# Kernel tuning notes

Hardware: AMD Instinct MI355X
Metric: run time of the kernel (lower is better)

## Reference

```python
import jax, jax.numpy as jnp
import numpy as np

N_NODES = 100000
N_EDGES = 1600000
N_FEAT = 128
HIDDEN = 64
N_CLASSES = 16


def setup_inputs() -> dict:
    key = jax.random.key(0)
    ks = jax.random.split(key, 8)
    x = jax.random.normal(ks[0], (N_NODES, N_FEAT), dtype=jnp.float32)
    edge_index = jax.random.randint(ks[1], (2, N_EDGES), 0, N_NODES, dtype=jnp.int64)
    def glorot(k, shape):
        lim = float(np.sqrt(6.0 / (shape[0] + shape[1])))
        return jax.random.uniform(k, shape, jnp.float32, -lim, lim)
    return {
        "x": x,
        "edge_index": edge_index,
        "W0": glorot(ks[2], (N_FEAT, HIDDEN)), "b0": jnp.zeros((HIDDEN,), jnp.float32),
        "W1": glorot(ks[3], (HIDDEN, HIDDEN)), "b1": jnp.zeros((HIDDEN,), jnp.float32),
        "W2": glorot(ks[4], (HIDDEN, 2)),      "b2": jnp.zeros((2,), jnp.float32),
        "Wc": glorot(ks[5], (2, N_CLASSES)),   "bc": jnp.zeros((N_CLASSES,), jnp.float32),
    }


def _gcn_conv(x, W, b, src, dst, norm, n_nodes):
    # GCNConv: D^{-1/2} (A + I) D^{-1/2} X W + b, edges already include self-loops
    h = x @ W                                  # transform first (small dim)
    msg = h[src] * norm[:, None]               # gather + per-edge scale
    agg = jax.ops.segment_sum(msg, dst, num_segments=n_nodes)  # scatter-add
    return agg + b


def reference(x, edge_index, W0, b0, W1, b1, W2, b2, Wc, bc):
    n = x.shape[0]
    loops = jnp.arange(n, dtype=edge_index.dtype)
    src = jnp.concatenate([edge_index[0], loops])
    dst = jnp.concatenate([edge_index[1], loops])
    # degree on destination (col), including self-loops
    deg = jax.ops.segment_sum(jnp.ones_like(dst, dtype=x.dtype), dst, num_segments=n)
    dis = jnp.where(deg > 0, jax.lax.rsqrt(deg), 0.0)
    norm = dis[src] * dis[dst]

    h = _gcn_conv(x, W0, b0, src, dst, norm, n)              # layer 0, no activation
    h = jnp.tanh(_gcn_conv(h, W1, b1, src, dst, norm, n))    # layer 1
    h = jnp.tanh(_gcn_conv(h, W2, b2, src, dst, norm, n))    # layer 2 -> [N, 2]
    embeddings = h
    out = embeddings @ Wc + bc                               # [N, num_classes]
    return (out, embeddings)
```

## Files before the change

kernel.cpp:

```cpp
#include <hip/hip_runtime.h>


#define NF 128
#define NH 64
#define NPB 256
#define MAXNB 512
#define CAP 6144
#define A1G 1024

typedef _Float16 half8 __attribute__((ext_vector_type(8)));
typedef float f32x4 __attribute__((ext_vector_type(4)));

__global__ void k_init0(const int* __restrict__ ei, int* __restrict__ fmt,
                        int* __restrict__ ccnt, int nb16) {
    int i = blockIdx.x * 256 + threadIdx.x;
    if (i < nb16) ccnt[i] = 0;
    if (i == 0) {
        int f = 1;
        #pragma unroll
        for (int k = 1; k < 32; k += 2) if (ei[k] != 0) f = 0;
        *fmt = f;
    }
}

__global__ void __launch_bounds__(256) k_coarse(
        const int* __restrict__ ei, const int* __restrict__ fmt,
        int* __restrict__ ccnt, int* __restrict__ blockbase, int E, int NB) {
    __shared__ int h[MAXNB];
    int sh = *fmt;
    for (int i = threadIdx.x; i < NB; i += 256) h[i] = 0;
    __syncthreads();
    for (long long e = (long long)blockIdx.x * 256 + threadIdx.x; e < E;
         e += (long long)A1G * 256) {
        int d = ei[(long long)(E + e) << sh];
        atomicAdd(&h[d >> 8], 1);
    }
    __syncthreads();
    for (int b = threadIdx.x; b < NB; b += 256) {
        int c = h[b];
        int base = (c > 0) ? atomicAdd(&ccnt[b * 16], c) : 0;
        blockbase[(long long)blockIdx.x * NB + b] = base;
    }
}

__global__ void __launch_bounds__(512) k_cscan(
        const int* __restrict__ ccnt, int* __restrict__ cstart, int NB) {
    __shared__ int s[512];
    int t = threadIdx.x;
    int c = (t < NB) ? ccnt[t * 16] : 0;
    s[t] = c;
    __syncthreads();
    for (int off = 1; off < 512; off <<= 1) {
        int v = s[t];
        int u = (t >= off) ? s[t - off] : 0;
        __syncthreads();
        s[t] = v + u;
        __syncthreads();
    }
    if (t < NB) cstart[t] = s[t] - c;
}

__global__ void __launch_bounds__(256) k_cscatter(
        const int* __restrict__ ei, const int* __restrict__ fmt,
        const int* __restrict__ cstart, const int* __restrict__ blockbase,
        int* __restrict__ pairs, int E, int NB) {
    __shared__ int h[MAXNB];
    __shared__ int bb[MAXNB];
    int sh = *fmt;
    for (int i = threadIdx.x; i < NB; i += 256) {
        h[i] = 0;
        bb[i] = cstart[i] + blockbase[(long long)blockIdx.x * NB + i];
    }
    __syncthreads();
    for (long long e = (long long)blockIdx.x * 256 + threadIdx.x; e < E;
         e += (long long)A1G * 256) {
        int s = ei[(long long)e << sh];
        int d = ei[(long long)(E + e) << sh];
        int b = d >> 8;
        int r = atomicAdd(&h[b], 1);
        pairs[bb[b] + r] = s | ((d & 255) << 17);
    }
}

__global__ void __launch_bounds__(256) k_bucket(
        const int* __restrict__ pairs, const int* __restrict__ ccnt,
        const int* __restrict__ cstart, int* __restrict__ esrc,
        int* __restrict__ cnt, int* __restrict__ start, float* __restrict__ dis,
        int N) {
    __shared__ int words[CAP];
    __shared__ unsigned char rk[CAP];
    __shared__ int h[NPB];
    __shared__ int hs[NPB];
    int b = blockIdx.x;
    int cs = cstart[b];
    int ec = ccnt[b * 16];
    if (ec > CAP) ec = CAP;
    int t = threadIdx.x;
    for (int i = t; i < ec; i += 256) words[i] = pairs[cs + i];
    h[t] = 0;
    __syncthreads();
    for (int i = t; i < ec; i += 256) {
        int ld = words[i] >> 17;
        rk[i] = (unsigned char)atomicAdd(&h[ld], 1);
    }
    __syncthreads();
    int c = h[t];
    hs[t] = c;
    __syncthreads();
    for (int off = 1; off < 256; off <<= 1) {
        int v = hs[t];
        int u = (t >= off) ? hs[t - off] : 0;
        __syncthreads();
        hs[t] = v + u;
        __syncthreads();
    }
    int node = b * NPB + t;
    if (node < N) {
        cnt[node] = c;
        start[node] = cs + hs[t] - c;
        dis[node] = rsqrtf(1.0f + (float)c);
    }
    for (int i = t; i < ec; i += 256) {
        int w = words[i];
        int ld = w >> 17;
        esrc[cs + (hs[ld] - h[ld]) + rk[i]] = w & 0x1FFFF;
    }
}

__global__ void k_wprep(const float* __restrict__ W, short* __restrict__ wf) {
    int b = blockIdx.x;
    int kc = b >> 2, ct = b & 3;
    int t = threadIdx.x;
    int lane = t & 63;
    int j0 = (t >> 6) * 2;
    #pragma unroll
    for (int jj = 0; jj < 2; ++jj) {
        int j = j0 + jj;
        int k = kc * 32 + (lane >> 4) * 8 + j;
        int col = ct * 16 + (lane & 15);
        float w = W[k * NH + col];
        _Float16 h = (_Float16)w;
        _Float16 l = (_Float16)(w - (float)h);
        int idx = (b * 64 + lane) * 8 + j;
        wf[idx] = *(short*)&h;
        wf[idx + 8192] = *(short*)&l;
    }
}

#define KPX 68
__global__ void __launch_bounds__(256) k_gemmM(
        const float* __restrict__ X, const short* __restrict__ wfrag,
        const float* __restrict__ dis, short* __restrict__ T16,
        float* __restrict__ rs, int n) {
    __shared__ __align__(16) short Wf[16384];
    __shared__ __align__(16) float xs[64 * KPX];
    int tid = threadIdx.x;
    {
        const int4* src = (const int4*)wfrag;
        int4* dst = (int4*)Wf;
        #pragma unroll
        for (int u = 0; u < 8; ++u) dst[tid + u * 256] = src[tid + u * 256];
    }
    long long rowbase = (long long)blockIdx.x * 64;
    int lane = tid & 63;
    int wid = tid >> 6;
    f32x4 acc0 = {0,0,0,0}, acc1 = {0,0,0,0}, acc2 = {0,0,0,0}, acc3 = {0,0,0,0};
    #pragma unroll
    for (int ph = 0; ph < 2; ++ph) {
        __syncthreads();
        const float* Xp = X + rowbase * NF + ph * 64;
        #pragma unroll
        for (int u = 0; u < 4; ++u) {
            int i = tid + u * 256;
            int r = i >> 4, kk = (i & 15) << 2;
            float4 v = (rowbase + r < n)
                           ? *(const float4*)(Xp + r * NF + kk)
                           : make_float4(0.f, 0.f, 0.f, 0.f);
            *(float4*)&xs[r * KPX + kk] = v;
        }
        __syncthreads();
        #pragma unroll
        for (int kcl = 0; kcl < 2; ++kcl) {
            const float* xp =
                &xs[(wid * 16 + (lane & 15)) * KPX + kcl * 32 + (lane >> 4) * 8];
            float4 xa = *(const float4*)xp;
            float4 xb = *(const float4*)(xp + 4);
            float xv[8] = {xa.x, xa.y, xa.z, xa.w, xb.x, xb.y, xb.z, xb.w};
            half8 ah, al;
            #pragma unroll
            for (int e = 0; e < 8; ++e) {
                _Float16 h = (_Float16)xv[e];
                ah[e] = h;
                al[e] = (_Float16)(xv[e] - (float)h);
            }
            int kc = ph * 2 + kcl;
            {
                const half8 bh = *(const half8*)&Wf[((kc * 4 + 0) * 64 + lane) * 8];
                const half8 bl = *(const half8*)&Wf[((kc * 4 + 0) * 64 + lane) * 8 + 8192];
                acc0 = __builtin_amdgcn_mfma_f32_16x16x32_f16(ah, bh, acc0, 0, 0, 0);
                acc0 = __builtin_amdgcn_mfma_f32_16x16x32_f16(ah, bl, acc0, 0, 0, 0);
                acc0 = __builtin_amdgcn_mfma_f32_16x16x32_f16(al, bh, acc0, 0, 0, 0);
            }
            {
                const half8 bh = *(const half8*)&Wf[((kc * 4 + 1) * 64 + lane) * 8];
                const half8 bl = *(const half8*)&Wf[((kc * 4 + 1) * 64 + lane) * 8 + 8192];
                acc1 = __builtin_amdgcn_mfma_f32_16x16x32_f16(ah, bh, acc1, 0, 0, 0);
                acc1 = __builtin_amdgcn_mfma_f32_16x16x32_f16(ah, bl, acc1, 0, 0, 0);
                acc1 = __builtin_amdgcn_mfma_f32_16x16x32_f16(al, bh, acc1, 0, 0, 0);
            }
            {
                const half8 bh = *(const half8*)&Wf[((kc * 4 + 2) * 64 + lane) * 8];
                const half8 bl = *(const half8*)&Wf[((kc * 4 + 2) * 64 + lane) * 8 + 8192];
                acc2 = __builtin_amdgcn_mfma_f32_16x16x32_f16(ah, bh, acc2, 0, 0, 0);
                acc2 = __builtin_amdgcn_mfma_f32_16x16x32_f16(ah, bl, acc2, 0, 0, 0);
                acc2 = __builtin_amdgcn_mfma_f32_16x16x32_f16(al, bh, acc2, 0, 0, 0);
            }
            {
                const half8 bh = *(const half8*)&Wf[((kc * 4 + 3) * 64 + lane) * 8];
                const half8 bl = *(const half8*)&Wf[((kc * 4 + 3) * 64 + lane) * 8 + 8192];
                acc3 = __builtin_amdgcn_mfma_f32_16x16x32_f16(ah, bh, acc3, 0, 0, 0);
                acc3 = __builtin_amdgcn_mfma_f32_16x16x32_f16(ah, bl, acc3, 0, 0, 0);
                acc3 = __builtin_amdgcn_mfma_f32_16x16x32_f16(al, bh, acc3, 0, 0, 0);
            }
        }
    }
    int rb = (int)rowbase + wid * 16 + (lane >> 4) * 4;
    float dr0 = (rb + 0 < n) ? dis[rb + 0] : 0.0f;
    float dr1 = (rb + 1 < n) ? dis[rb + 1] : 0.0f;
    float dr2 = (rb + 2 < n) ? dis[rb + 2] : 0.0f;
    float dr3 = (rb + 3 < n) ? dis[rb + 3] : 0.0f;
    float drs[4] = {dr0, dr1, dr2, dr3};
    const float ks = 1.0f / 32767.0f;
    int cb = lane & 15;
    #pragma unroll
    for (int r = 0; r < 4; ++r) {
        float v0 = acc0[r] * drs[r];
        float v1 = acc1[r] * drs[r];
        float v2 = acc2[r] * drs[r];
        float v3 = acc3[r] * drs[r];
        float m = fmaxf(fmaxf(fabsf(v0), fabsf(v1)), fmaxf(fabsf(v2), fabsf(v3)));
        m = fmaxf(m, __shfl_xor(m, 1, 64));
        m = fmaxf(m, __shfl_xor(m, 2, 64));
        m = fmaxf(m, __shfl_xor(m, 4, 64));
        m = fmaxf(m, __shfl_xor(m, 8, 64));
        float ir = 32767.0f / fmaxf(m, 1e-20f);
        int rowg = rb + r;
        if (rowg < n) {
            long long base = (long long)rowg * NH;
            T16[base + 0  + cb] = (short)__float2int_rn(v0 * ir);
            T16[base + 16 + cb] = (short)__float2int_rn(v1 * ir);
            T16[base + 32 + cb] = (short)__float2int_rn(v2 * ir);
            T16[base + 48 + cb] = (short)__float2int_rn(v3 * ir);
            if (cb == 0) rs[rowg] = m * ks;
        }
    }
}

#define EDGE_A(J) {                                                           \
    int s_ = __builtin_amdgcn_readlane(sA, (J));                              \
    float f_ = __int_as_float(__builtin_amdgcn_readlane(fAb, (J)));           \
    accA = fmaf(f_, (float)(T + s_ * NH)[lane], accA); }
#define EDGE_B(J) {                                                           \
    int s_ = __builtin_amdgcn_readlane(sB, (J));                              \
    float f_ = __int_as_float(__builtin_amdgcn_readlane(fBb, (J)));           \
    accB = fmaf(f_, (float)(T + s_ * NH)[lane], accB); }

#define SEG_GATHER2                                                           \
    int lane = threadIdx.x & 63;                                              \
    int na = blockIdx.x * 8 + (threadIdx.x >> 6) * 2;                         \
    int nb_ = na + 1;                                                         \
    if (na >= n) return;                                                      \
    bool hasB = (nb_ < n);                                                    \
    float dia = dis[na];                                                      \
    float dib = hasB ? dis[nb_] : 0.0f;                                       \
    int ga = cnt[na], sta = start[na];                                        \
    int gb = hasB ? cnt[nb_] : 0;                                             \
    int stb = hasB ? start[nb_] : 0;                                          \
    float accA = rs[na] * (float)T[na * NH + lane];                           \
    float accB = hasB ? rs[nb_] * (float)T[nb_ * NH + lane] : 0.0f;           \
    int gmax = ga > gb ? ga : gb;                                             \
    for (int base = 0; base < gmax; base += 64) {                             \
        int ma = ga - base; ma = ma < 0 ? 0 : (ma > 64 ? 64 : ma);            \
        int mb = gb - base; mb = mb < 0 ? 0 : (mb > 64 ? 64 : mb);            \
        int sA = 0, sB = 0; float fA = 0.0f, fB = 0.0f;                       \
        if (lane < ma) { sA = esrc[sta + base + lane]; fA = rs[sA]; }         \
        if (lane < mb) { sB = esrc[stb + base + lane]; fB = rs[sB]; }         \
        int fAb = __float_as_int(fA), fBb = __float_as_int(fB);               \
        int mmin = ma < mb ? ma : mb;                                         \
        int j = 0;                                                            \
        for (; j + 3 < mmin; j += 4) {                                        \
            EDGE_A(j + 0) EDGE_B(j + 0)                                       \
            EDGE_A(j + 1) EDGE_B(j + 1)                                       \
            EDGE_A(j + 2) EDGE_B(j + 2)                                       \
            EDGE_A(j + 3) EDGE_B(j + 3)                                       \
        }                                                                     \
        int jA = j, jB = j;                                                   \
        for (; jA + 3 < ma; jA += 4) {                                        \
            EDGE_A(jA + 0) EDGE_A(jA + 1) EDGE_A(jA + 2) EDGE_A(jA + 3)       \
        }                                                                     \
        for (; jA < ma; ++jA) EDGE_A(jA)                                      \
        for (; jB + 3 < mb; jB += 4) {                                        \
            EDGE_B(jB + 0) EDGE_B(jB + 1) EDGE_B(jB + 2) EDGE_B(jB + 3)       \
        }                                                                     \
        for (; jB < mb; ++jB) EDGE_B(jB)                                      \
    }

__global__ void __launch_bounds__(256) k_seg0t(
        const short* __restrict__ T, const float* __restrict__ rs,
        const int* __restrict__ esrc, const int* __restrict__ start,
        const int* __restrict__ cnt, const float* __restrict__ dis,
        const float* __restrict__ b0, const float* __restrict__ W1,
        short* __restrict__ To, float* __restrict__ rso, int n) {
    __shared__ float W1s[NH * NH];
    for (int i = threadIdx.x; i < NH * NH / 4; i += 256)
        ((float4*)W1s)[i] = ((const float4*)W1)[i];
    __syncthreads();
    SEG_GATHER2
    float bv = b0[lane];
    float hA = dia * accA + bv;
    float hB = dib * accB + bv;
    float oA0 = 0.0f, oA1 = 0.0f, oB0 = 0.0f, oB1 = 0.0f;
    #pragma unroll
    for (int c = 0; c < 64; c += 2) {
        float wv0 = W1s[(c + 0) * NH + lane];
        float wv1 = W1s[(c + 1) * NH + lane];
        float ha0 = __int_as_float(__builtin_amdgcn_readlane(__float_as_int(hA), c + 0));
        float ha1 = __int_as_float(__builtin_amdgcn_readlane(__float_as_int(hA), c + 1));
        float hb0 = __int_as_float(__builtin_amdgcn_readlane(__float_as_int(hB), c + 0));
        float hb1 = __int_as_float(__builtin_amdgcn_readlane(__float_as_int(hB), c + 1));
        oA0 = fmaf(ha0, wv0, oA0);
        oA1 = fmaf(ha1, wv1, oA1);
        oB0 = fmaf(hb0, wv0, oB0);
        oB1 = fmaf(hb1, wv1, oB1);
    }
    float oA = (oA0 + oA1) * dia;
    float oB = (oB0 + oB1) * dib;
    float mA = fabsf(oA), mB = fabsf(oB);
    #pragma unroll
    for (int msk = 32; msk; msk >>= 1) {
        mA = fmaxf(mA, __shfl_xor(mA, msk, 64));
        mB = fmaxf(mB, __shfl_xor(mB, msk, 64));
    }
    float iA = 32767.0f / fmaxf(mA, 1e-20f);
    float iB = 32767.0f / fmaxf(mB, 1e-20f);
    const float ks = 1.0f / 32767.0f;
    To[(long long)na * NH + lane] = (short)__float2int_rn(oA * iA);
    if (lane == 0) rso[na] = mA * ks;
    if (hasB) {
        To[(long long)nb_ * NH + lane] = (short)__float2int_rn(oB * iB);
        if (lane == 0) rso[nb_] = mB * ks;
    }
}

__global__ void __launch_bounds__(256) k_seg1f(
        const short* __restrict__ T, const float* __restrict__ rs,
        const int* __restrict__ esrc, const int* __restrict__ start,
        const int* __restrict__ cnt, const float* __restrict__ dis,
        const float* __restrict__ b1, const float* __restrict__ W2,
        float2* __restrict__ t2, int n) {
    SEG_GATHER2
    float bv = b1[lane];
    float2 w = ((const float2*)W2)[lane];
    float tA = tanhf(dia * accA + bv);
    float p0 = tA * w.x, p1 = tA * w.y;
    float tB = hasB ? tanhf(dib * accB + bv) : 0.0f;
    float q0 = tB * w.x, q1 = tB * w.y;
    #pragma unroll
    for (int msk = 32; msk; msk >>= 1) {
        p0 += __shfl_xor(p0, msk, 64);
        p1 += __shfl_xor(p1, msk, 64);
        q0 += __shfl_xor(q0, msk, 64);
        q1 += __shfl_xor(q1, msk, 64);
    }
    if (lane == 0) {
        t2[na] = make_float2(dia * p0, dia * p1);
        if (hasB) t2[nb_] = make_float2(dib * q0, dib * q1);
    }
}

__global__ void __launch_bounds__(256) k_seg2f(
        const float2* __restrict__ T2, const int* __restrict__ esrc,
        const int* __restrict__ start, const int* __restrict__ cnt,
        const float* __restrict__ dis, const float* __restrict__ b2,
        const float* __restrict__ Wc, const float* __restrict__ bc,
        float* __restrict__ out, float* __restrict__ emb, int n) {
    int lane = threadIdx.x & 63;
    int sub = lane >> 4;
    int sl = lane & 15;
    int i = blockIdx.x * 16 + (threadIdx.x >> 6) * 4 + sub;
    if (i >= n) return;
    float di = dis[i];
    int g = cnt[i], st = start[i];
    float a0 = 0.0f, a1 = 0.0f;
    for (int j = sl; j < g; j += 16) {
        float2 v = T2[esrc[st + j]];
        a0 += v.x; a1 += v.y;
    }
    if (sl == 0) {
        float2 s = T2[i];
        a0 += s.x; a1 += s.y;
    }
    #pragma unroll
    for (int msk = 8; msk; msk >>= 1) {
        a0 += __shfl_xor(a0, msk, 64);
        a1 += __shfl_xor(a1, msk, 64);
    }
    float e0 = tanhf(a0 * di + b2[0]);
    float e1 = tanhf(a1 * di + b2[1]);
    if (sl == 0) *(float2*)&emb[(long long)i * 2] = make_float2(e0, e1);
    if (sl < 4) {
        int c = sl * 4;
        float4 o;
        o.x = e0 * Wc[c + 0] + e1 * Wc[16 + c + 0] + bc[c + 0];
        o.y = e0 * Wc[c + 1] + e1 * Wc[16 + c + 1] + bc[c + 1];
        o.z = e0 * Wc[c + 2] + e1 * Wc[16 + c + 2] + bc[c + 2];
        o.w = e0 * Wc[c + 3] + e1 * Wc[16 + c + 3] + bc[c + 3];
        *(float4*)&out[(long long)i * 16 + c] = o;
    }
}

extern "C" void kernel_launch(void* const* d_in, const int* in_sizes, int n_in,
                              void* d_out, int out_size, void* d_ws, size_t ws_size,
                              hipStream_t stream) {
    const float* x  = (const float*)d_in[0];
    const int*   ei = (const int*)  d_in[1];
    const float* W0 = (const float*)d_in[2];
    const float* b0 = (const float*)d_in[3];
    const float* W1 = (const float*)d_in[4];
    const float* b1 = (const float*)d_in[5];
    const float* W2 = (const float*)d_in[6];
    const float* b2 = (const float*)d_in[7];
    const float* Wc = (const float*)d_in[8];
    const float* bc = (const float*)d_in[9];

    int N = in_sizes[0] / NF;
    int E = in_sizes[1] / 2;
    int NB = (N + NPB - 1) / NPB;

    float* out = (float*)d_out;
    float* emb = out + (long long)N * 16;

    short*  T16a = (short*)d_ws;
    char*   r2   = (char*)d_ws + (long long)N * NH * 2;
    short*  T16b = (short*)r2;
    short*  wfrag = (short*)r2;
    float2* t2   = (float2*)(r2 + (long long)N * NH * 2);
    float*  rs_b = (float*)(r2 + (long long)N * NH * 2 + (long long)N * 8);
    float*  dis  = (float*)((char*)d_ws + (long long)N * NH * 2 + (long long)N * NH * 4);
    float*  rs_a = dis + N;
    int*    cnt   = (int*)(rs_a + N);
    int*    start = cnt + N;
    int*    esrc  = start + N;
    int*    fmt   = esrc + E;

    int* pairs     = (int*)d_ws;
    int* blockbase = pairs + E;
    int* ccnt      = blockbase + (long long)A1G * NB;
    int* cstart    = ccnt + NB * 16;

    int nb_g  = (N + 63) / 64;
    int nb_s2 = (N + 7) / 8;
    int nb_2f = (N + 15) / 16;
    int nb_i0 = (NB * 16 + 255) / 256;

    k_wprep   <<<16, 256, 0, stream>>>(W0, wfrag);

    k_init0   <<<nb_i0, 256, 0, stream>>>(ei, fmt, ccnt, NB * 16);
    k_coarse  <<<A1G, 256, 0, stream>>>(ei, fmt, ccnt, blockbase, E, NB);
    k_cscan   <<<1, 512, 0, stream>>>(ccnt, cstart, NB);
    k_cscatter<<<A1G, 256, 0, stream>>>(ei, fmt, cstart, blockbase, pairs, E, NB);
    k_bucket  <<<NB, 256, 0, stream>>>(pairs, ccnt, cstart, esrc, cnt, start, dis, N);

    k_gemmM   <<<nb_g, 256, 0, stream>>>(x, wfrag, dis, T16a, rs_a, N);

    k_seg0t   <<<nb_s2, 256, 0, stream>>>(T16a, rs_a, esrc, start, cnt, dis, b0,
                                          W1, T16b, rs_b, N);

    k_seg1f   <<<nb_s2, 256, 0, stream>>>(T16b, rs_b, esrc, start, cnt, dis, b1,
                                          W2, t2, N);

    k_seg2f   <<<nb_2f, 256, 0, stream>>>(t2, esrc, start, cnt, dis, b2, Wc, bc,
                                          out, emb, N);
}
```

Measured before the change: 316.8 us.

## Split layer-1 transform out of segment kernel into MFMA GEMM

The layer-0 aggregation kernel no longer performs the 64x64 W1 transform with scalar readlane FMAs; it now writes fp32 aggregated features, and a new split-fp16 MFMA GEMM kernel applies W1, scales by dis and quantizes to int16. The layer-0 GEMM also drops its shared-memory staging of X and loads A fragments directly from global memory. This swaps per-lane scalar FMA work for tensor-core throughput, at the cost of an extra kernel launch and an N×64 fp32 round trip through memory. Weight fragments are staged in the output buffer.

```diff
diff --git a/kernel.cpp b/kernel.cpp
--- a/kernel.cpp
+++ b/kernel.cpp
@@ -127,12 +127,17 @@
     }
 }
 
-__global__ void k_wprep(const float* __restrict__ W, short* __restrict__ wf) {
+__global__ void k_wprep(const float* __restrict__ W0, const float* __restrict__ W1,
+                        short* __restrict__ wf0, short* __restrict__ wf1) {
     int b = blockIdx.x;
-    int kc = b >> 2, ct = b & 3;
     int t = threadIdx.x;
     int lane = t & 63;
     int j0 = (t >> 6) * 2;
+    const float* W = (b < 16) ? W0 : W1;
+    int bb = (b < 16) ? b : (b - 16);
+    short* wf = (b < 16) ? wf0 : wf1;
+    int lohalf = (b < 16) ? 8192 : 4096;
+    int kc = bb >> 2, ct = bb & 3;
     #pragma unroll
     for (int jj = 0; jj < 2; ++jj) {
         int j = j0 + jj;
@@ -141,19 +146,70 @@
         float w = W[k * NH + col];
         _Float16 h = (_Float16)w;
         _Float16 l = (_Float16)(w - (float)h);
-        int idx = (b * 64 + lane) * 8 + j;
+        int idx = (bb * 64 + lane) * 8 + j;
         wf[idx] = *(short*)&h;
-        wf[idx + 8192] = *(short*)&l;
-    }
-}
-
-#define KPX 68
+        wf[idx + lohalf] = *(short*)&l;
+    }
+}
+
+#define GEMM_EPILOGUE                                                         \
+    int rb = (int)rowbase + wid * 16 + (lane >> 4) * 4;                       \
+    float drs[4];                                                             \
+    drs[0] = (rb + 0 < n) ? dis[rb + 0] : 0.0f;                               \
+    drs[1] = (rb + 1 < n) ? dis[rb + 1] : 0.0f;                               \
+    drs[2] = (rb + 2 < n) ? dis[rb + 2] : 0.0f;                               \
+    drs[3] = (rb + 3 < n) ? dis[rb + 3] : 0.0f;                               \
+    const float ks = 1.0f / 32767.0f;                                         \
+    int cb = lane & 15;                                                       \
+    _Pragma("unroll")                                                         \
+    for (int r = 0; r < 4; ++r) {                                             \
+        float v0 = acc0[r] * drs[r];                                          \
+        float v1 = acc1[r] * drs[r];                                          \
+        float v2 = acc2[r] * drs[r];                                          \
+        float v3 = acc3[r] * drs[r];                                          \
+        float m = fmaxf(fmaxf(fabsf(v0), fabsf(v1)), fmaxf(fabsf(v2), fabsf(v3))); \
+        m = fmaxf(m, __shfl_xor(m, 1, 64));                                   \
+        m = fmaxf(m, __shfl_xor(m, 2, 64));                                   \
+        m = fmaxf(m, __shfl_xor(m, 4, 64));                                   \
+        m = fmaxf(m, __shfl_xor(m, 8, 64));                                   \
+        float ir = 32767.0f / fmaxf(m, 1e-20f);                               \
+        int rowg = rb + r;                                                    \
+        if (rowg < n) {                                                       \
+            long long base = (long long)rowg * NH;                            \
+            T16[base + 0  + cb] = (short)__float2int_rn(v0 * ir);             \
+            T16[base + 16 + cb] = (short)__float2int_rn(v1 * ir);             \
+            T16[base + 32 + cb] = (short)__float2int_rn(v2 * ir);             \
+            T16[base + 48 + cb] = (short)__float2int_rn(v3 * ir);             \
+            if (cb == 0) rs[rowg] = m * ks;                                   \
+        }                                                                     \
+    }
+
+#define CVT_AFRAG(xa, xb4)                                                    \
+    half8 ah, al;                                                             \
+    {                                                                         \
+        float xv[8] = {xa.x, xa.y, xa.z, xa.w, xb4.x, xb4.y, xb4.z, xb4.w};   \
+        _Pragma("unroll")                                                     \
+        for (int e = 0; e < 8; ++e) {                                         \
+            _Float16 h = (_Float16)xv[e];                                     \
+            ah[e] = h;                                                        \
+            al[e] = (_Float16)(xv[e] - (float)h);                             \
+        }                                                                     \
+    }
+
+#define MFMA3(ACC, SETIDX, LOHALF)                                            \
+    {                                                                         \
+        const half8 bh = *(const half8*)&Wf[((SETIDX) * 64 + lane) * 8];      \
+        const half8 bl = *(const half8*)&Wf[((SETIDX) * 64 + lane) * 8 + (LOHALF)]; \
+        ACC = __builtin_amdgcn_mfma_f32_16x16x32_f16(ah, bh, ACC, 0, 0, 0);   \
+        ACC = __builtin_amdgcn_mfma_f32_16x16x32_f16(ah, bl, ACC, 0, 0, 0);   \
+        ACC = __builtin_amdgcn_mfma_f32_16x16x32_f16(al, bh, ACC, 0, 0, 0);   \
+    }
+
 __global__ void __launch_bounds__(256) k_gemmM(
         const float* __restrict__ X, const short* __restrict__ wfrag,
         const float* __restrict__ dis, short* __restrict__ T16,
         float* __restrict__ rs, int n) {
     __shared__ __align__(16) short Wf[16384];
-    __shared__ __align__(16) float xs[64 * KPX];
     int tid = threadIdx.x;
     {
         const int4* src = (const int4*)wfrag;
@@ -161,99 +217,62 @@
         #pragma unroll
         for (int u = 0; u < 8; ++u) dst[tid + u * 256] = src[tid + u * 256];
     }
+    __syncthreads();
     long long rowbase = (long long)blockIdx.x * 64;
     int lane = tid & 63;
     int wid = tid >> 6;
+    int row = (int)rowbase + wid * 16 + (lane & 15);
+    bool ok = row < n;
+    const float* xb = X + (long long)row * NF + (lane >> 4) * 8;
     f32x4 acc0 = {0,0,0,0}, acc1 = {0,0,0,0}, acc2 = {0,0,0,0}, acc3 = {0,0,0,0};
     #pragma unroll
-    for (int ph = 0; ph < 2; ++ph) {
-        __syncthreads();
-        const float* Xp = X + rowbase * NF + ph * 64;
+    for (int kc = 0; kc < 4; ++kc) {
+        float4 xa = ok ? *(const float4*)(xb + kc * 32)
+                       : make_float4(0.f, 0.f, 0.f, 0.f);
+        float4 xc = ok ? *(const float4*)(xb + kc * 32 + 4)
+                       : make_float4(0.f, 0.f, 0.f, 0.f);
+        CVT_AFRAG(xa, xc)
+        MFMA3(acc0, kc * 4 + 0, 8192)
+        MFMA3(acc1, kc * 4 + 1, 8192)
+        MFMA3(acc2, kc * 4 + 2, 8192)
+        MFMA3(acc3, kc * 4 + 3, 8192)
+    }
+    GEMM_EPILOGUE
+}
+
+__global__ void __launch_bounds__(256) k_gemmM64(
+        const float* __restrict__ H, const short* __restrict__ wfrag,
+        const float* __restrict__ dis, short* __restrict__ T16,
+        float* __restrict__ rs, int n) {
+    __shared__ __align__(16) short Wf[8192];
+    int tid = threadIdx.x;
+    {
+        const int4* src = (const int4*)wfrag;
+        int4* dst = (int4*)Wf;
         #pragma unroll
-        for (int u = 0; u < 4; ++u) {
-            int i = tid + u * 256;
-            int r = i >> 4, kk = (i & 15) << 2;
-            float4 v = (rowbase + r < n)
-                           ? *(const float4*)(Xp + r * NF + kk)
-                           : make_float4(0.f, 0.f, 0.f, 0.f);
-            *(float4*)&xs[r * KPX + kk] = v;
-        }
-        __syncthreads();
-        #pragma unroll
-        for (int kcl = 0; kcl < 2; ++kcl) {
-            const float* xp =
-                &xs[(wid * 16 + (lane & 15)) * KPX + kcl * 32 + (lane >> 4) * 8];
-            float4 xa = *(const float4*)xp;
-            float4 xb = *(const float4*)(xp + 4);
-            float xv[8] = {xa.x, xa.y, xa.z, xa.w, xb.x, xb.y, xb.z, xb.w};
-            half8 ah, al;
-            #pragma unroll
-            for (int e = 0; e < 8; ++e) {
-                _Float16 h = (_Float16)xv[e];
-                ah[e] = h;
-                al[e] = (_Float16)(xv[e] - (float)h);
-            }
-            int kc = ph * 2 + kcl;
-            {
-                const half8 bh = *(const half8*)&Wf[((kc * 4 + 0) * 64 + lane) * 8];
-                const half8 bl = *(const half8*)&Wf[((kc * 4 + 0) * 64 + lane) * 8 + 8192];
-                acc0 = __builtin_amdgcn_mfma_f32_16x16x32_f16(ah, bh, acc0, 0, 0, 0);
-                acc0 = __builtin_amdgcn_mfma_f32_16x16x32_f16(ah, bl, acc0, 0, 0, 0);
-                acc0 = __builtin_amdgcn_mfma_f32_16x16x32_f16(al, bh, acc0, 0, 0, 0);
-            }
-            {
-                const half8 bh = *(const half8*)&Wf[((kc * 4 + 1) * 64 + lane) * 8];
-                const half8 bl = *(const half8*)&Wf[((kc * 4 + 1) * 64 + lane) * 8 + 8192];
-                acc1 = __builtin_amdgcn_mfma_f32_16x16x32_f16(ah, bh, acc1, 0, 0, 0);
-                acc1 = __builtin_amdgcn_mfma_f32_16x16x32_f16(ah, bl, acc1, 0, 0, 0);
-                acc1 = __builtin_amdgcn_mfma_f32_16x16x32_f16(al, bh, acc1, 0, 0, 0);
-            }
-            {
-                const half8 bh = *(const half8*)&Wf[((kc * 4 + 2) * 64 + lane) * 8];
-                const half8 bl = *(const half8*)&Wf[((kc * 4 + 2) * 64 + lane) * 8 + 8192];
-                acc2 = __builtin_amdgcn_mfma_f32_16x16x32_f16(ah, bh, acc2, 0, 0, 0);
-                acc2 = __builtin_amdgcn_mfma_f32_16x16x32_f16(ah, bl, acc2, 0, 0, 0);
-                acc2 = __builtin_amdgcn_mfma_f32_16x16x32_f16(al, bh, acc2, 0, 0, 0);
-            }
-            {
-                const half8 bh = *(const half8*)&Wf[((kc * 4 + 3) * 64 + lane) * 8];
-                const half8 bl = *(const half8*)&Wf[((kc * 4 + 3) * 64 + lane) * 8 + 8192];
-                acc3 = __builtin_amdgcn_mfma_f32_16x16x32_f16(ah, bh, acc3, 0, 0, 0);
-                acc3 = __builtin_amdgcn_mfma_f32_16x16x32_f16(ah, bl, acc3, 0, 0, 0);
-                acc3 = __builtin_amdgcn_mfma_f32_16x16x32_f16(al, bh, acc3, 0, 0, 0);
-            }
-        }
-    }
-    int rb = (int)rowbase + wid * 16 + (lane >> 4) * 4;
-    float dr0 = (rb + 0 < n) ? dis[rb + 0] : 0.0f;
-    float dr1 = (rb + 1 < n) ? dis[rb + 1] : 0.0f;
-    float dr2 = (rb + 2 < n) ? dis[rb + 2] : 0.0f;
-    float dr3 = (rb + 3 < n) ? dis[rb + 3] : 0.0f;
-    float drs[4] = {dr0, dr1, dr2, dr3};
-    const float ks = 1.0f / 32767.0f;
-    int cb = lane & 15;
+        for (int u = 0; u < 4; ++u) dst[tid + u * 256] = src[tid + u * 256];
+    }
+    __syncthreads();
+    long long rowbase = (long long)blockIdx.x * 64;
+    int lane = tid & 63;
+    int wid = tid >> 6;
+    int row = (int)rowbase + wid * 16 + (lane & 15);
+    bool ok = row < n;
+    const float* hb = H + (long long)row * NH + (lane >> 4) * 8;
+    f32x4 acc0 = {0,0,0,0}, acc1 = {0,0,0,0}, acc2 = {0,0,0,0}, acc3 = {0,0,0,0};
     #pragma unroll
-    for (int r = 0; r < 4; ++r) {
-        float v0 = acc0[r] * drs[r];
-        float v1 = acc1[r] * drs[r];
-        float v2 = acc2[r] * drs[r];
-        float v3 = acc3[r] * drs[r];
-        float m = fmaxf(fmaxf(fabsf(v0), fabsf(v1)), fmaxf(fabsf(v2), fabsf(v3)));
-        m = fmaxf(m, __shfl_xor(m, 1, 64));
-        m = fmaxf(m, __shfl_xor(m, 2, 64));
-        m = fmaxf(m, __shfl_xor(m, 4, 64));
-        m = fmaxf(m, __shfl_xor(m, 8, 64));
-        float ir = 32767.0f / fmaxf(m, 1e-20f);
-        int rowg = rb + r;
-        if (rowg < n) {
-            long long base = (long long)rowg * NH;
-            T16[base + 0  + cb] = (short)__float2int_rn(v0 * ir);
-            T16[base + 16 + cb] = (short)__float2int_rn(v1 * ir);
-            T16[base + 32 + cb] = (short)__float2int_rn(v2 * ir);
-            T16[base + 48 + cb] = (short)__float2int_rn(v3 * ir);
-            if (cb == 0) rs[rowg] = m * ks;
-        }
-    }
+    for (int kc = 0; kc < 2; ++kc) {
+        float4 xa = ok ? *(const float4*)(hb + kc * 32)
+                       : make_float4(0.f, 0.f, 0.f, 0.f);
+        float4 xc = ok ? *(const float4*)(hb + kc * 32 + 4)
+                       : make_float4(0.f, 0.f, 0.f, 0.f);
+        CVT_AFRAG(xa, xc)
+        MFMA3(acc0, kc * 4 + 0, 4096)
+        MFMA3(acc1, kc * 4 + 1, 4096)
+        MFMA3(acc2, kc * 4 + 2, 4096)
+        MFMA3(acc3, kc * 4 + 3, 4096)
+    }
+    GEMM_EPILOGUE
 }
 
 #define EDGE_A(J) {                                                           \
@@ -305,51 +324,15 @@
         for (; jB < mb; ++jB) EDGE_B(jB)                                      \
     }
 
-__global__ void __launch_bounds__(256) k_seg0t(
+__global__ void __launch_bounds__(256) k_seg(
         const short* __restrict__ T, const float* __restrict__ rs,
         const int* __restrict__ esrc, const int* __restrict__ start,
         const int* __restrict__ cnt, const float* __restrict__ dis,
-        const float* __restrict__ b0, const float* __restrict__ W1,
-        short* __restrict__ To, float* __restrict__ rso, int n) {
-    __shared__ float W1s[NH * NH];
-    for (int i = threadIdx.x; i < NH * NH / 4; i += 256)
-        ((float4*)W1s)[i] = ((const float4*)W1)[i];
-    __syncthreads();
+        const float* __restrict__ b0, float* __restrict__ O, int n) {
     SEG_GATHER2
     float bv = b0[lane];
-    float hA = dia * accA + bv;
-    float hB = dib * accB + bv;
-    float oA0 = 0.0f, oA1 = 0.0f, oB0 = 0.0f, oB1 = 0.0f;
-    #pragma unroll
-    for (int c = 0; c < 64; c += 2) {
-        float wv0 = W1s[(c + 0) * NH + lane];
-        float wv1 = W1s[(c + 1) * NH + lane];
-        float ha0 = __int_as_float(__builtin_amdgcn_readlane(__float_as_int(hA), c + 0));
-        float ha1 = __int_as_float(__builtin_amdgcn_readlane(__float_as_int(hA), c + 1));
-        float hb0 = __int_as_float(__builtin_amdgcn_readlane(__float_as_int(hB), c + 0));
-        float hb1 = __int_as_float(__builtin_amdgcn_readlane(__float_as_int(hB), c + 1));
-        oA0 = fmaf(ha0, wv0, oA0);
-        oA1 = fmaf(ha1, wv1, oA1);
-        oB0 = fmaf(hb0, wv0, oB0);
-        oB1 = fmaf(hb1, wv1, oB1);
-    }
-    float oA = (oA0 + oA1) * dia;
-    float oB = (oB0 + oB1) * dib;
-    float mA = fabsf(oA), mB = fabsf(oB);
-    #pragma unroll
-    for (int msk = 32; msk; msk >>= 1) {
-        mA = fmaxf(mA, __shfl_xor(mA, msk, 64));
-        mB = fmaxf(mB, __shfl_xor(mB, msk, 64));
-    }
-    float iA = 32767.0f / fmaxf(mA, 1e-20f);
-    float iB = 32767.0f / fmaxf(mB, 1e-20f);
-    const float ks = 1.0f / 32767.0f;
-    To[(long long)na * NH + lane] = (short)__float2int_rn(oA * iA);
-    if (lane == 0) rso[na] = mA * ks;
-    if (hasB) {
-        To[(long long)nb_ * NH + lane] = (short)__float2int_rn(oB * iB);
-        if (lane == 0) rso[nb_] = mB * ks;
-    }
+    O[(long long)na * NH + lane] = dia * accA + bv;
+    if (hasB) O[(long long)nb_ * NH + lane] = dib * accB + bv;
 }
 
 __global__ void __launch_bounds__(256) k_seg1f(
@@ -441,17 +424,16 @@
     float* emb = out + (long long)N * 16;
 
     short*  T16a = (short*)d_ws;
-    char*   r2   = (char*)d_ws + (long long)N * NH * 2;
-    short*  T16b = (short*)r2;
-    short*  wfrag = (short*)r2;
-    float2* t2   = (float2*)(r2 + (long long)N * NH * 2);
-    float*  rs_b = (float*)(r2 + (long long)N * NH * 2 + (long long)N * 8);
+    float*  Bb   = (float*)((char*)d_ws + (long long)N * NH * 2);
     float*  dis  = (float*)((char*)d_ws + (long long)N * NH * 2 + (long long)N * NH * 4);
     float*  rs_a = dis + N;
     int*    cnt   = (int*)(rs_a + N);
     int*    start = cnt + N;
     int*    esrc  = start + N;
     int*    fmt   = esrc + E;
+    short*  wf0   = (short*)d_out;
+    short*  wf1   = wf0 + 16384;
+    float2* t2    = (float2*)Bb;
 
     int* pairs     = (int*)d_ws;
     int* blockbase = pairs + E;
@@ -463,7 +445,7 @@
     int nb_2f = (N + 15) / 16;
     int nb_i0 = (NB * 16 + 255) / 256;
 
-    k_wprep   <<<16, 256, 0, stream>>>(W0, wfrag);
+    k_wprep   <<<24, 256, 0, stream>>>(W0, W1, wf0, wf1);
 
     k_init0   <<<nb_i0, 256, 0, stream>>>(ei, fmt, ccnt, NB * 16);
     k_coarse  <<<A1G, 256, 0, stream>>>(ei, fmt, ccnt, blockbase, E, NB);
@@ -471,12 +453,14 @@
     k_cscatter<<<A1G, 256, 0, stream>>>(ei, fmt, cstart, blockbase, pairs, E, NB);
     k_bucket  <<<NB, 256, 0, stream>>>(pairs, ccnt, cstart, esrc, cnt, start, dis, N);
 
-    k_gemmM   <<<nb_g, 256, 0, stream>>>(x, wfrag, dis, T16a, rs_a, N);
-
-    k_seg0t   <<<nb_s2, 256, 0, stream>>>(T16a, rs_a, esrc, start, cnt, dis, b0,
-                                          W1, T16b, rs_b, N);
-
-    k_seg1f   <<<nb_s2, 256, 0, stream>>>(T16b, rs_b, esrc, start, cnt, dis, b1,
+    k_gemmM   <<<nb_g, 256, 0, stream>>>(x, wf0, dis, T16a, rs_a, N);
+
+    k_seg     <<<nb_s2, 256, 0, stream>>>(T16a, rs_a, esrc, start, cnt, dis, b0,
+                                          Bb, N);
+
+    k_gemmM64 <<<nb_g, 256, 0, stream>>>(Bb, wf1, dis, T16a, rs_a, N);
+
+    k_seg1f   <<<nb_s2, 256, 0, stream>>>(T16a, rs_a, esrc, start, cnt, dis, b1,
                                           W2, t2, N);
 
     k_seg2f   <<<nb_2f, 256, 0, stream>>>(t2, esrc, start, cnt, dis, b2, Wc, bc,
```

New measurement: 303.6 us. 1.04x faster.
